# Kernel tuning notes

Hardware: AMD Instinct MI355X
Metric: run time of the kernel (lower is better)

The kernel has to match this reference:

```python
import jax, jax.numpy as jnp
import numpy as np

N_EMBD = 1024
N_HEAD = 16
HEAD_DIM = N_EMBD // N_HEAD


def setup_inputs() -> dict:
    key = jax.random.key(0)
    kx, kq, kk, kv, ko = jax.random.split(key, 5)
    s = 1.0 / np.sqrt(N_EMBD)
    return {
        "x": jax.random.normal(kx, (4, 2048, N_EMBD), dtype=jnp.float32),
        "Wq": jax.random.normal(kq, (N_EMBD, N_EMBD), dtype=jnp.float32) * s,
        "Wk": jax.random.normal(kk, (N_EMBD, N_EMBD), dtype=jnp.float32) * s,
        "Wv": jax.random.normal(kv, (N_EMBD, N_EMBD), dtype=jnp.float32) * s,
        "Wo": jax.random.normal(ko, (N_EMBD, N_EMBD), dtype=jnp.float32) * s,
    }


def reference(x, Wq, Wk, Wv, Wo):
    B, T, C = x.shape
    H, D = N_HEAD, HEAD_DIM
    # projections; torch Linear computes x @ W.T
    q = (x @ Wq.T).reshape(B, T, H, D).transpose(0, 2, 1, 3)  # [B,H,T,D]
    k = (x @ Wk.T).reshape(B, T, H, D).transpose(0, 2, 1, 3)
    v = (x @ Wv.T).reshape(B, T, H, D).transpose(0, 2, 1, 3)
    scores = jnp.einsum("bhtd,bhsd->bhts", q, k) / np.sqrt(D).astype(np.float32)
    causal = jnp.tril(jnp.ones((T, T), dtype=bool))
    scores = jnp.where(causal, scores, -jnp.inf)
    attn = jax.nn.softmax(scores, axis=-1)
    out = jnp.einsum("bhts,bhsd->bhtd", attn, v)  # [B,H,T,D]
    out = out.transpose(0, 2, 1, 3).reshape(B, T, C)
    return out @ Wo.T
```

## Files before the change

kernel.cpp:

```cpp
#include <hip/hip_runtime.h>
#include <hip/hip_bf16.h>


typedef __bf16 bf16_t;
typedef __bf16 bf16x4 __attribute__((ext_vector_type(4)));
typedef __bf16 bf16x8 __attribute__((ext_vector_type(8)));
typedef float  f32x4  __attribute__((ext_vector_type(4)));

#define MFMA16(a, b, c) __builtin_amdgcn_mfma_f32_16x16x32_bf16(a, b, c, 0, 0, 0)

__device__ __forceinline__ float exp2_(float x) {
#if __has_builtin(__builtin_amdgcn_exp2f)
    return __builtin_amdgcn_exp2f(x);
#else
    return __expf(x * 0.6931471805599453f);
#endif
}

__device__ __forceinline__ void gload_lds16(const bf16_t* g, bf16_t* l) {
    __builtin_amdgcn_global_load_lds(
        (const __attribute__((address_space(1))) void*)g,
        (__attribute__((address_space(3))) void*)l, 16, 0, 0);
}

__global__ __launch_bounds__(256)
void cast_all(const float* __restrict__ x,  const float* __restrict__ Wq,
              const float* __restrict__ Wk, const float* __restrict__ Wv,
              const float* __restrict__ Wo,
              bf16_t* __restrict__ xb, bf16_t* __restrict__ wqkv,
              bf16_t* __restrict__ wob) {
    int i = blockIdx.x * 256 + threadIdx.x;
    const float* src;
    bf16_t* dst;
    if (blockIdx.y == 0) {
        src = x; dst = xb;
    } else {
        if (i >= 524288) return;
        int wsel = i >> 17;
        int loc  = i & 131071;
        src = wsel == 0 ? Wq : wsel == 1 ? Wk : wsel == 2 ? Wv : Wo;
        dst = wsel == 3 ? wob : wqkv + (size_t)wsel * 1048576;
        i = loc;
    }
    const float4* p = (const float4*)src;
    float4 a = p[i * 2], b = p[i * 2 + 1];
    bf16x8 o;
    o[0] = (bf16_t)a.x; o[1] = (bf16_t)a.y; o[2] = (bf16_t)a.z; o[3] = (bf16_t)a.w;
    o[4] = (bf16_t)b.x; o[5] = (bf16_t)b.y; o[6] = (bf16_t)b.z; o[7] = (bf16_t)b.w;
    *(bf16x8*)(dst + (size_t)i * 8) = o;
}

__device__ __forceinline__ void mfma16x(f32x4 (*acc)[4], int m0,
                                        bf16x8 a00, bf16x8 a01,
                                        bf16x8 a10, bf16x8 a11,
                                        const bf16x8 bfr[4][2]) {
    #pragma unroll
    for (int n = 0; n < 4; ++n) {
        acc[m0][n]     = MFMA16(a00, bfr[n][0], acc[m0][n]);
        acc[m0][n]     = MFMA16(a01, bfr[n][1], acc[m0][n]);
        acc[m0 + 1][n] = MFMA16(a10, bfr[n][0], acc[m0 + 1][n]);
        acc[m0 + 1][n] = MFMA16(a11, bfr[n][1], acc[m0 + 1][n]);
    }
}

__global__ __launch_bounds__(512, 2)
void gemm_8ph(const bf16_t* __restrict__ A, const bf16_t* __restrict__ B,
              bf16_t* __restrict__ C, int M, int N, int K) {
    __shared__ bf16_t sm[2][2][256 * 64];
    const int tid = threadIdx.x;
    const int lane = tid & 63, w = tid >> 6;
    const int wr = w >> 2, wc = w & 3;
    const int g = lane >> 4, c = lane & 15;
    const long bm = (long)blockIdx.x * 256;
    const long bn = (long)blockIdx.y * 256;

    const int srow8 = tid >> 3;
    const int pb = tid & 7;

    auto STAGE_H = [&](int buf, int op, int h, int kt) {
        const bf16_t* base = op ? B + bn * (long)K : A + bm * (long)K;
        #pragma unroll
        for (int r = 0; r < 2; ++r) {
            int row = h * 128 + r * 64 + srow8;
            int lb  = pb ^ (row & 7);
            gload_lds16(base + (long)row * K + kt * 64 + lb * 8,
                        &sm[buf][op][row * 64 + pb * 8]);
        }
    };
    auto LDA = [&](int buf, int m, int k) -> bf16x8 {
        int row = wr * 128 + m * 16 + c;
        return *(const bf16x8*)&sm[buf][0][row * 64 + (((k * 4 + g) ^ (row & 7)) * 8)];
    };
    auto LDB = [&](int buf, int n, int k) -> bf16x8 {
        int row = wc * 64 + n * 16 + c;
        return *(const bf16x8*)&sm[buf][1][row * 64 + (((k * 4 + g) ^ (row & 7)) * 8)];
    };

#define PHASE(BUF, M0, ISSUE_STMT, WAIT_STMT)                          \
    {                                                                  \
        bf16x8 a00 = LDA(BUF, M0, 0),     a01 = LDA(BUF, M0, 1);       \
        bf16x8 a10 = LDA(BUF, M0 + 1, 0), a11 = LDA(BUF, M0 + 1, 1);   \
        ISSUE_STMT;                                                    \
        WAIT_STMT;                                                     \
        __builtin_amdgcn_s_barrier();                                  \
        asm volatile("s_waitcnt lgkmcnt(0)" ::: "memory");             \
        __builtin_amdgcn_sched_barrier(0);                             \
        __builtin_amdgcn_s_setprio(1);                                 \
        mfma16x(acc, M0, a00, a01, a10, a11, bfr);                     \
        __builtin_amdgcn_s_setprio(0);                                 \
        __builtin_amdgcn_s_barrier();                                  \
    }

    f32x4 acc[8][4] = {};
    bf16x8 bfr[4][2];
    const int NJ = K / 128;

    STAGE_H(0, 1, 0, 0); STAGE_H(0, 1, 1, 0);
    STAGE_H(0, 0, 0, 0); STAGE_H(0, 0, 1, 0);
    STAGE_H(1, 1, 0, 1); STAGE_H(1, 1, 1, 1);
    asm volatile("s_waitcnt vmcnt(4)" ::: "memory");
    __builtin_amdgcn_s_barrier();

    for (int j = 0; j < NJ; ++j) {
        const int t0 = 2 * j;
        const bool more = (j + 1 < NJ);

        #pragma unroll
        for (int n = 0; n < 4; ++n) { bfr[n][0] = LDB(0, n, 0); bfr[n][1] = LDB(0, n, 1); }
        PHASE(0, 0, STAGE_H(1, 0, 0, t0 + 1), (void)0);
        PHASE(0, 2, STAGE_H(1, 0, 1, t0 + 1), (void)0);
        PHASE(0, 4, if (more) STAGE_H(0, 1, 0, t0 + 2), (void)0);
        PHASE(0, 6, if (more) STAGE_H(0, 1, 1, t0 + 2),
              if (more) { asm volatile("s_waitcnt vmcnt(4)" ::: "memory"); }
              else      { asm volatile("s_waitcnt vmcnt(0)" ::: "memory"); });

        #pragma unroll
        for (int n = 0; n < 4; ++n) { bfr[n][0] = LDB(1, n, 0); bfr[n][1] = LDB(1, n, 1); }
        PHASE(1, 0, if (more) STAGE_H(0, 0, 0, t0 + 2), (void)0);
        PHASE(1, 2, if (more) STAGE_H(0, 0, 1, t0 + 2), (void)0);
        PHASE(1, 4, if (more) STAGE_H(1, 1, 0, t0 + 3), (void)0);
        PHASE(1, 6, if (more) STAGE_H(1, 1, 1, t0 + 3),
              if (more) { asm volatile("s_waitcnt vmcnt(4)" ::: "memory"); });
    }
#undef PHASE

    #pragma unroll
    for (int m = 0; m < 8; ++m)
        #pragma unroll
        for (int n = 0; n < 4; ++n)
            #pragma unroll
            for (int i = 0; i < 4; ++i) {
                long row = bm + wr * 128 + m * 16 + g * 4 + i;
                long col = bn + wc * 64 + n * 16 + c;
                C[row * N + col] = (bf16_t)acc[m][n][i];
            }
}

template<int OUT_BF16>
__global__ __launch_bounds__(256)
void gemm_bt64(const bf16_t* __restrict__ A, const bf16_t* __restrict__ B,
               void* __restrict__ Cv, int M, int N, int K) {
    __shared__ bf16_t As[128 * 64];
    __shared__ bf16_t Bs[128 * 64];
    const int tid = threadIdx.x;
    const int lane = tid & 63;
    const int w = tid >> 6;
    const int wm = w >> 1, wn = w & 1;
    const int g = lane >> 4, c = lane & 15;
    const long bm = (long)blockIdx.x * 128;
    const long bn = (long)blockIdx.y * 128;

    f32x4 acc[4][4] = {};

    const int srow = tid >> 3;
    const int scb  = tid & 7;
    bf16_t* AsW = As + tid * 8;
    bf16_t* BsW = Bs + tid * 8;

    for (int k0 = 0; k0 < K; k0 += 64) {
        #pragma unroll
        for (int r = 0; r < 4; ++r) {
            int row = r * 32 + srow;
            int lb  = scb ^ (row & 7);
            gload_lds16(A + (bm + row) * (long)K + k0 + lb * 8, AsW + r * 2048);
            gload_lds16(B + (bn + row) * (long)K + k0 + lb * 8, BsW + r * 2048);
        }
        __syncthreads();
        bf16x8 bfr[4][2];
        #pragma unroll
        for (int n = 0; n < 4; ++n) {
            const int row = wn * 64 + n * 16 + c;
            #pragma unroll
            for (int ks = 0; ks < 2; ++ks)
                bfr[n][ks] = *(const bf16x8*)(Bs + row * 64 +
                                 (((ks * 4 + g) ^ (row & 7)) * 8));
        }
        #pragma unroll
        for (int m = 0; m < 4; ++m) {
            const int row = wm * 64 + m * 16 + c;
            bf16x8 af0 = *(const bf16x8*)(As + row * 64 + ((g       ^ (row & 7)) * 8));
            bf16x8 af1 = *(const bf16x8*)(As + row * 64 + (((4 + g) ^ (row & 7)) * 8));
            #pragma unroll
            for (int n = 0; n < 4; ++n) {
                acc[m][n] = MFMA16(af0, bfr[n][0], acc[m][n]);
                acc[m][n] = MFMA16(af1, bfr[n][1], acc[m][n]);
            }
        }
        __syncthreads();
    }
    #pragma unroll
    for (int m = 0; m < 4; ++m)
        #pragma unroll
        for (int n = 0; n < 4; ++n)
            #pragma unroll
            for (int i = 0; i < 4; ++i) {
                long row = bm + wm * 64 + m * 16 + g * 4 + i;
                long col = bn + wn * 64 + n * 16 + c;
                float v = acc[m][n][i];
                if (OUT_BF16) ((bf16_t*)Cv)[row * N + col] = (bf16_t)v;
                else          ((float*)Cv)[row * N + col]  = v;
            }
}

__device__ __forceinline__ void stage_K(const bf16_t* Kp, long rowb, int kb, int hcol,
                                        bf16_t* Kbuf, int tid) {
    int row = tid >> 3;
    int lb  = (tid & 7) ^ (row & 7);
    gload_lds16(Kp + (rowb + kb + row) * 3072 + hcol + lb * 8, Kbuf + tid * 8);
}

__device__ __forceinline__ bf16x8 load_V8(const bf16_t* Vp, long rowb, int kb,
                                          int hcol, int tid) {
    const int d  = tid & 63;
    const int k0 = (tid >> 6) * 8;
    bf16x8 v;
    #pragma unroll
    for (int j = 0; j < 8; ++j)
        v[j] = Vp[(rowb + kb + k0 + j) * 3072 + hcol + d];
    return v;
}

__device__ __forceinline__ void write_V8(bf16_t* Vbuf, int tid, bf16x8 v) {
    const int d  = tid & 63;
    const int k0 = (tid >> 6) * 8;
    *(bf16x8*)&Vbuf[d * 72 + k0] = v;
}

__global__ __launch_bounds__(512, 6)
void attn_kernel(const bf16_t* __restrict__ Qp, const bf16_t* __restrict__ Kp,
                 const bf16_t* __restrict__ Vp, bf16_t* __restrict__ O) {
    __shared__ bf16_t Ks[2][64 * 64];
    __shared__ bf16_t Vts[2][64 * 72];
    __shared__ bf16_t PW[8][16 * 72];

    const int tid = threadIdx.x, lane = tid & 63, w = tid >> 6;
    const int g = lane >> 4, c = lane & 15;
    const int bh = blockIdx.x;
    const int b = bh >> 4, h = bh & 15;
    const long rowb = (long)b * 2048;
    const int hcol = h * 64;
    const float QSCL = 0.18033688011112042f;

    const int q0  = 15 - blockIdx.y;
    const int qlo = q0 * 128 + w * 16;
    const int nkt = 2 * q0 + 2;

    bf16x8 qf[2];
    #pragma unroll
    for (int ks = 0; ks < 2; ++ks) {
        qf[ks] = *(const bf16x8*)(Qp + (rowb + qlo + c) * 3072 +
                                  hcol + ks * 32 + g * 8);
        #pragma unroll
        for (int j = 0; j < 8; ++j)
            qf[ks][j] = (bf16_t)((float)qf[ks][j] * QSCL);
    }

    float m_r = -1e30f;
    float l_r = 0.f;
    f32x4 acc[4] = {};

    stage_K(Kp, rowb, 0, hcol, Ks[0], tid);
    write_V8(Vts[0], tid, load_V8(Vp, rowb, 0, hcol, tid));
    __syncthreads();

    for (int t = 0; t < nkt; ++t) {
        const int cur = t & 1;
        const int kb = t * 64;
        const bool pre = (t + 1 < nkt);
        bf16x8 vreg;
        if (pre) {
            stage_K(Kp, rowb, kb + 64, hcol, Ks[cur ^ 1], tid);
            vreg = load_V8(Vp, rowb, kb + 64, hcol, tid);
        }

        if (kb <= qlo + 15) {
            f32x4 sacc[4] = {};
            __builtin_amdgcn_s_setprio(1);
            #pragma unroll
            for (int nt = 0; nt < 4; ++nt) {
                const int row = nt * 16 + c;
                #pragma unroll
                for (int ks = 0; ks < 2; ++ks) {
                    bf16x8 kf = *(const bf16x8*)&Ks[cur][row * 64 +
                                    (((ks * 4 + g) ^ (c & 7)) * 8)];
                    sacc[nt] = MFMA16(kf, qf[ks], sacc[nt]);
                }
            }
            __builtin_amdgcn_s_setprio(0);
            if (kb + 63 > qlo) {
                const int q = qlo + c;
                #pragma unroll
                for (int nt = 0; nt < 4; ++nt)
                    #pragma unroll
                    for (int i = 0; i < 4; ++i) {
                        int key = kb + nt * 16 + g * 4 + i;
                        if (key > q) sacc[nt][i] = -1e30f;
                    }
            }

            float m0 = fmaxf(fmaxf(sacc[0][0], sacc[0][1]),
                             fmaxf(fmaxf(sacc[0][2], sacc[0][3]), sacc[1][0]));
            float m1 = fmaxf(fmaxf(sacc[1][1], sacc[1][2]),
                             fmaxf(fmaxf(sacc[1][3], sacc[2][0]), sacc[2][1]));
            float m2 = fmaxf(fmaxf(sacc[2][2], sacc[2][3]),
                             fmaxf(fmaxf(sacc[3][0], sacc[3][1]),
                                   fmaxf(sacc[3][2], sacc[3][3])));
            float mx = fmaxf(fmaxf(m0, m1), m2);
            if (__any(mx > m_r + 8.f)) {
                mx = fmaxf(mx, __shfl_xor(mx, 16, 64));
                mx = fmaxf(mx, __shfl_xor(mx, 32, 64));
                float mnew = fmaxf(m_r, mx);
                float scl = exp2_(m_r - mnew);
                #pragma unroll
                for (int nt = 0; nt < 4; ++nt)
                    acc[nt] *= scl;
                l_r *= scl;
                m_r = mnew;
            }
            float rsn[4];
            #pragma unroll
            for (int nt = 0; nt < 4; ++nt) {
                #pragma unroll
                for (int i = 0; i < 4; ++i)
                    sacc[nt][i] = exp2_(sacc[nt][i] - m_r);
                rsn[nt] = (sacc[nt][0] + sacc[nt][1]) + (sacc[nt][2] + sacc[nt][3]);
            }
            l_r += (rsn[0] + rsn[1]) + (rsn[2] + rsn[3]);

            #pragma unroll
            for (int nt = 0; nt < 4; ++nt) {
                bf16x4 t4;
                #pragma unroll
                for (int i = 0; i < 4; ++i) t4[i] = (bf16_t)sacc[nt][i];
                *(bf16x4*)&PW[w][c * 72 + nt * 16 + g * 4] = t4;
            }

            __builtin_amdgcn_s_setprio(1);
            #pragma unroll
            for (int ks = 0; ks < 2; ++ks) {
                bf16x8 pf = *(const bf16x8*)&PW[w][c * 72 + ks * 32 + g * 8];
                #pragma unroll
                for (int nt = 0; nt < 4; ++nt) {
                    bf16x8 vf = *(const bf16x8*)&Vts[cur][(nt * 16 + c) * 72 +
                                                          ks * 32 + g * 8];
                    acc[nt] = MFMA16(vf, pf, acc[nt]);
                }
            }
            __builtin_amdgcn_s_setprio(0);
        }

        if (pre) write_V8(Vts[cur ^ 1], tid, vreg);
        __syncthreads();
    }

    l_r += __shfl_xor(l_r, 16, 64);
    l_r += __shfl_xor(l_r, 32, 64);
    {
        float rl = __builtin_amdgcn_rcpf(l_r);
        #pragma unroll
        for (int nt = 0; nt < 4; ++nt) {
            bf16x4 t4;
            #pragma unroll
            for (int i = 0; i < 4; ++i) t4[i] = (bf16_t)(acc[nt][i] * rl);
            *(bf16x4*)&PW[w][c * 72 + nt * 16 + g * 4] = t4;
        }
    }
    #pragma unroll
    for (int p = 0; p < 2; ++p) {
        int row = p * 8 + (lane >> 3);
        int ch  = (lane & 7) * 8;
        bf16x8 v = *(const bf16x8*)&PW[w][row * 72 + ch];
        *(bf16x8*)&O[(rowb + qlo + row) * 1024 + hcol + ch] = v;
    }
}

extern "C" void kernel_launch(void* const* d_in, const int* in_sizes, int n_in,
                              void* d_out, int out_size, void* d_ws, size_t ws_size,
                              hipStream_t stream) {
    const float* x  = (const float*)d_in[0];
    const float* Wq = (const float*)d_in[1];
    const float* Wk = (const float*)d_in[2];
    const float* Wv = (const float*)d_in[3];
    const float* Wo = (const float*)d_in[4];

    const int M = 8192;
    const int C = 1024;

    char* ws = (char*)d_ws;
    bf16_t* xb   = (bf16_t*)(ws);
    bf16_t* wqkv = (bf16_t*)(ws + ((size_t)16 << 20));
    bf16_t* wob  = (bf16_t*)(ws + ((size_t)22 << 20));
    bf16_t* qkv  = (bf16_t*)(ws + ((size_t)24 << 20));
    bf16_t* aob  = (bf16_t*)(ws + ((size_t)72 << 20));

    cast_all<<<dim3(4096, 2), 256, 0, stream>>>(x, Wq, Wk, Wv, Wo, xb, wqkv, wob);

    gemm_8ph<<<dim3(M / 256, 3072 / 256), 512, 0, stream>>>(xb, wqkv, qkv, M, 3072, C);

    attn_kernel<<<dim3(64, 16), 512, 0, stream>>>(
        qkv, qkv + 1024, qkv + 2048, aob);

    gemm_bt64<0><<<dim3(M / 128, C / 128), 256, 0, stream>>>(aob, wob, d_out, M, C, C);
}
```

Before: 165.1 us.

## Stage V via async global-to-LDS loads and read with transpose LDS instructions

The V tile used to be loaded as scalar strided global reads into registers and then written transposed into LDS. It is now copied directly into LDS with global_load_lds in row-major order with an XOR swizzle, and the transposed MFMA operands are read with ds_read_b64_tr_b16. This removes the uncoalesced 2-byte global loads and the register round trip. In exchange the kernel relies on hand-written inline asm, explicit waitcnt and sched barriers, and a carefully computed swizzle that must match the transpose-read addressing.

Result: slower. 185.5 us (+12.3%).

```diff
diff --git a/kernel.cpp b/kernel.cpp
--- a/kernel.cpp
+++ b/kernel.cpp
@@ -222,6 +222,7 @@
             }
 }
 
+
 __device__ __forceinline__ void stage_K(const bf16_t* Kp, long rowb, int kb, int hcol,
                                         bf16_t* Kbuf, int tid) {
     int row = tid >> 3;
@@ -229,29 +230,25 @@
     gload_lds16(Kp + (rowb + kb + row) * 3072 + hcol + lb * 8, Kbuf + tid * 8);
 }
 
-__device__ __forceinline__ bf16x8 load_V8(const bf16_t* Vp, long rowb, int kb,
-                                          int hcol, int tid) {
-    const int d  = tid & 63;
-    const int k0 = (tid >> 6) * 8;
-    bf16x8 v;
-    #pragma unroll
-    for (int j = 0; j < 8; ++j)
-        v[j] = Vp[(rowb + kb + k0 + j) * 3072 + hcol + d];
-    return v;
-}
-
-__device__ __forceinline__ void write_V8(bf16_t* Vbuf, int tid, bf16x8 v) {
-    const int d  = tid & 63;
-    const int k0 = (tid >> 6) * 8;
-    *(bf16x8*)&Vbuf[d * 72 + k0] = v;
-}
+__device__ __forceinline__ void stage_Vtr(const bf16_t* Vp, long rowb, int kb, int hcol,
+                                          bf16_t* Vbuf, int tid) {
+    const int k = tid >> 3;
+    const int p = tid & 7;
+    const int dq0 = (2 * p) ^ ((k & 3) * 4);
+    gload_lds16(Vp + (rowb + kb + k) * 3072 + hcol + dq0 * 4, Vbuf + tid * 8);
+}
+
+#define TRD(dst, va, OFF) \
+    asm volatile("ds_read_b64_tr_b16 %0, %1 offset:" OFF : "=&v"(dst) : "v"(va))
+#define COMB(vf, lo, hi) \
+    { union { uint4 u; bf16x8 b; } _c; _c.u = make_uint4(lo.x, lo.y, hi.x, hi.y); vf = _c.b; }
 
 __global__ __launch_bounds__(512, 6)
 void attn_kernel(const bf16_t* __restrict__ Qp, const bf16_t* __restrict__ Kp,
                  const bf16_t* __restrict__ Vp, bf16_t* __restrict__ O) {
-    __shared__ bf16_t Ks[2][64 * 64];
-    __shared__ bf16_t Vts[2][64 * 72];
-    __shared__ bf16_t PW[8][16 * 72];
+    __shared__ __align__(16) bf16_t Ks[2][64 * 64];
+    __shared__ __align__(16) bf16_t Vtr[2][64 * 64];
+    __shared__ __align__(16) bf16_t PW[8][16 * 72];
 
     const int tid = threadIdx.x, lane = tid & 63, w = tid >> 6;
     const int g = lane >> 4, c = lane & 15;
@@ -265,6 +262,14 @@
     const int qlo = q0 * 128 + w * 16;
     const int nkt = 2 * q0 + 2;
 
+    const unsigned vbase =
+        (unsigned)(size_t)(__attribute__((address_space(3))) bf16_t*)&Vtr[0][0];
+    const unsigned vrow = (unsigned)((g * 8 + (c >> 2)) * 128 + (c & 3) * 8);
+    const unsigned va0 = vbase + vrow + ((0u ^ (unsigned)(c >> 2)) * 32);
+    const unsigned va1 = vbase + vrow + ((1u ^ (unsigned)(c >> 2)) * 32);
+    const unsigned va2 = vbase + vrow + ((2u ^ (unsigned)(c >> 2)) * 32);
+    const unsigned va3 = vbase + vrow + ((3u ^ (unsigned)(c >> 2)) * 32);
+
     bf16x8 qf[2];
     #pragma unroll
     for (int ks = 0; ks < 2; ++ks) {
@@ -280,17 +285,15 @@
     f32x4 acc[4] = {};
 
     stage_K(Kp, rowb, 0, hcol, Ks[0], tid);
-    write_V8(Vts[0], tid, load_V8(Vp, rowb, 0, hcol, tid));
+    stage_Vtr(Vp, rowb, 0, hcol, Vtr[0], tid);
     __syncthreads();
 
     for (int t = 0; t < nkt; ++t) {
         const int cur = t & 1;
         const int kb = t * 64;
-        const bool pre = (t + 1 < nkt);
-        bf16x8 vreg;
-        if (pre) {
+        if (t + 1 < nkt) {
             stage_K(Kp, rowb, kb + 64, hcol, Ks[cur ^ 1], tid);
-            vreg = load_V8(Vp, rowb, kb + 64, hcol, tid);
+            stage_Vtr(Vp, rowb, kb + 64, hcol, Vtr[cur ^ 1], tid);
         }
 
         if (kb <= qlo + 15) {
@@ -307,6 +310,16 @@
                 }
             }
             __builtin_amdgcn_s_setprio(0);
+
+            const unsigned co = (unsigned)(cur * 8192);
+            const unsigned vat0 = va0 + co, vat1 = va1 + co,
+                           vat2 = va2 + co, vat3 = va3 + co;
+            uint2 r0l, r0h, r1l, r1h, r2l, r2h, r3l, r3h;
+            TRD(r0l, vat0, "0"); TRD(r0h, vat0, "512");
+            TRD(r1l, vat1, "0"); TRD(r1h, vat1, "512");
+            TRD(r2l, vat2, "0"); TRD(r2h, vat2, "512");
+            TRD(r3l, vat3, "0"); TRD(r3h, vat3, "512");
+
             if (kb + 63 > qlo) {
                 const int q = qlo + c;
                 #pragma unroll
@@ -355,21 +368,36 @@
                 *(bf16x4*)&PW[w][c * 72 + nt * 16 + g * 4] = t4;
             }
 
+            bf16x8 pf0 = *(const bf16x8*)&PW[w][c * 72 + g * 8];
+            bf16x8 vf0, vf1, vf2, vf3;
+            COMB(vf0, r0l, r0h); COMB(vf1, r1l, r1h);
+            COMB(vf2, r2l, r2h); COMB(vf3, r3l, r3h);
+            asm volatile("s_waitcnt lgkmcnt(0)" ::: "memory");
+            __builtin_amdgcn_sched_barrier(0);
             __builtin_amdgcn_s_setprio(1);
-            #pragma unroll
-            for (int ks = 0; ks < 2; ++ks) {
-                bf16x8 pf = *(const bf16x8*)&PW[w][c * 72 + ks * 32 + g * 8];
-                #pragma unroll
-                for (int nt = 0; nt < 4; ++nt) {
-                    bf16x8 vf = *(const bf16x8*)&Vts[cur][(nt * 16 + c) * 72 +
-                                                          ks * 32 + g * 8];
-                    acc[nt] = MFMA16(vf, pf, acc[nt]);
-                }
-            }
+            acc[0] = MFMA16(vf0, pf0, acc[0]);
+            acc[1] = MFMA16(vf1, pf0, acc[1]);
+            acc[2] = MFMA16(vf2, pf0, acc[2]);
+            acc[3] = MFMA16(vf3, pf0, acc[3]);
             __builtin_amdgcn_s_setprio(0);
-        }
-
-        if (pre) write_V8(Vts[cur ^ 1], tid, vreg);
+
+            TRD(r0l, vat0, "4096"); TRD(r0h, vat0, "4608");
+            TRD(r1l, vat1, "4096"); TRD(r1h, vat1, "4608");
+            TRD(r2l, vat2, "4096"); TRD(r2h, vat2, "4608");
+            TRD(r3l, vat3, "4096"); TRD(r3h, vat3, "4608");
+            bf16x8 pf1 = *(const bf16x8*)&PW[w][c * 72 + 32 + g * 8];
+            COMB(vf0, r0l, r0h); COMB(vf1, r1l, r1h);
+            COMB(vf2, r2l, r2h); COMB(vf3, r3l, r3h);
+            asm volatile("s_waitcnt lgkmcnt(0)" ::: "memory");
+            __builtin_amdgcn_sched_barrier(0);
+            __builtin_amdgcn_s_setprio(1);
+            acc[0] = MFMA16(vf0, pf1, acc[0]);
+            acc[1] = MFMA16(vf1, pf1, acc[1]);
+            acc[2] = MFMA16(vf2, pf1, acc[2]);
+            acc[3] = MFMA16(vf3, pf1, acc[3]);
+            __builtin_amdgcn_s_setprio(0);
+        }
+
         __syncthreads();
     }
 
```
